# Optimization experiments

Hardware: AMD Instinct MI355X
Metric: run time of the kernel (lower is better)

Reference implementation:

```python
import jax, jax.numpy as jnp
import numpy as np

IN_FEATURES = 64 * 64 * 3  # 12288, hard-coded in the torch module

# Sign with straight-through estimator (BinaryNet-style): fwd = sign(x),
# bwd = grad * 1{|x| <= 1} (hardtanh clip).
@jax.custom_vjp
def ste_sign(x):
    return jnp.sign(x)

def _ste_fwd(x):
    return jnp.sign(x), x

def _ste_bwd(x, g):
    return (g * (jnp.abs(x) <= 1.0).astype(g.dtype),)

ste_sign.defvjp(_ste_fwd, _ste_bwd)


def setup_inputs() -> dict:
    key = jax.random.key(0)
    k1, k2 = jax.random.split(key)
    B, C = 8192, 1000
    inp = jax.random.normal(k1, (B, IN_FEATURES), dtype=jnp.float32)
    # Linear weight init scale ~ U(-1/sqrt(fan_in), 1/sqrt(fan_in)); use scaled normal
    weight = jax.random.normal(k2, (C, IN_FEATURES), dtype=jnp.float32) * (1.0 / np.sqrt(IN_FEATURES))
    return {"input": inp, "weight": weight}


def reference(input, weight):
    x = input.reshape(-1, IN_FEATURES)
    # F.linear(sign(x), sign(W)) = sign(x) @ sign(W)^T  -> [B, num_classes]
    return jnp.einsum("bd,cd->bc", ste_sign(x), ste_sign(weight))
```

## Files before the change

### kernel.cpp

```cpp
#include <hip/hip_runtime.h>
#include <hip/hip_bf16.h>


#define K_DIM   12288
#define N_CLS   1000
#define N_PAD   1024
#define KSPLIT  2
#define K_HALF  (K_DIM / KSPLIT)
#define STAGE_BYTES (N_PAD * 64)
#define N_STAGE_TOT (K_DIM / 64)
#define CHUNK_STAGES 2
#define CHUNK_K  (CHUNK_STAGES * 64)
#define CHUNKS   (K_HALF / CHUNK_K)
#define M_TILE   64
#define B_ROWS   8192
#define WS_W_BYTES ((size_t)N_STAGE_TOT * STAGE_BYTES)
#define WS_P_BYTES ((size_t)B_ROWS * N_CLS * 4)

typedef int int4v __attribute__((ext_vector_type(4)));
typedef unsigned int uint4v __attribute__((ext_vector_type(4)));

__device__ __forceinline__ unsigned sign_byte(unsigned bits) {
    unsigned mag = bits & 0x7fffffffu;
    unsigned nz = mag ? 1u : 0u;
    int sgn = ((int)bits) >> 31;
    int v = (((int)nz) ^ sgn) - sgn;
    return (unsigned)(v & 0xff);
}

__device__ __forceinline__ unsigned pack4(uint4v b) {
    return sign_byte(b.x) | (sign_byte(b.y) << 8) |
           (sign_byte(b.z) << 16) | (sign_byte(b.w) << 24);
}

__global__ void pack_w_kernel(const float* __restrict__ w,
                              unsigned char* __restrict__ ws) {
    const int gid = blockIdx.x * 256 + threadIdx.x;
    const int stage = gid >> 12;
    const int n = (gid >> 2) & 1023;
    const int q16 = gid & 3;
    const int k = stage * 64 + q16 * 16;
    uint4v o = {0u, 0u, 0u, 0u};
    if (n < N_CLS) {
        const float* p = w + (size_t)n * K_DIM + k;
        o.x = pack4(*reinterpret_cast<const uint4v*>(p));
        o.y = pack4(*reinterpret_cast<const uint4v*>(p + 4));
        o.z = pack4(*reinterpret_cast<const uint4v*>(p + 8));
        o.w = pack4(*reinterpret_cast<const uint4v*>(p + 12));
    }
    *reinterpret_cast<uint4v*>(ws + (size_t)stage * STAGE_BYTES + n * 64 + q16 * 16) = o;
}

__global__ void zero_kernel(float* __restrict__ out) {
    const int i = blockIdx.x * 256 + threadIdx.x;
    float4 z = {0.f, 0.f, 0.f, 0.f};
    *reinterpret_cast<float4*>(out + (size_t)i * 4) = z;
}

__global__ void reduce_kernel(const unsigned* __restrict__ part,
                              float* __restrict__ out) {
    const int i = blockIdx.x * 256 + threadIdx.x;
    uint4v w = *reinterpret_cast<const uint4v*>(part + (size_t)i * 4);
    float4 f;
    f.x = (float)((int)(short)(w.x & 0xffffu) + (int)(short)(w.x >> 16));
    f.y = (float)((int)(short)(w.y & 0xffffu) + (int)(short)(w.y >> 16));
    f.z = (float)((int)(short)(w.z & 0xffffu) + (int)(short)(w.z >> 16));
    f.w = (float)((int)(short)(w.w & 0xffffu) + (int)(short)(w.w >> 16));
    *reinterpret_cast<float4*>(out + (size_t)i * 4) = f;
}

template<int USE_PARTIAL>
__global__ __launch_bounds__(512, 2)
void bgemm_kernel(const float* __restrict__ x,
                  const unsigned char* __restrict__ wq,
                  unsigned* __restrict__ part,
                  float* __restrict__ out) {
    __shared__ unsigned x_lds[2][M_TILE * 32];

    const int tid  = threadIdx.x;
    const int wave = tid >> 6;
    const int lane = tid & 63;
    const int q    = lane >> 4;
    const int l15  = lane & 15;
    const int bx   = blockIdx.x;
    const int mtile = bx >> 1;
    const int kh    = bx & 1;
    const int m0    = mtile * M_TILE;
    const int nbase = wave * 128;

    int4v acc[4][8];
#pragma unroll
    for (int i = 0; i < 4; ++i)
#pragma unroll
        for (int j = 0; j < 8; ++j)
            acc[i][j] = (int4v){0, 0, 0, 0};

    const int srow = tid >> 3;
    const int scol = tid & 7;
    const float* xp = x + (size_t)(m0 + srow) * K_DIM + kh * K_HALF + scol * 4;
    const int sw_w = (srow & 3) * 8;

    const unsigned char* wqb = wq + (size_t)(kh * (N_STAGE_TOT / KSPLIT)) * STAGE_BYTES
                               + (nbase + l15) * 64 + q * 16;
    const int rsw = (l15 & 3) * 8;

    uint4v xr[4];
#pragma unroll
    for (int i = 0; i < 4; ++i)
        xr[i] = __builtin_nontemporal_load(reinterpret_cast<const uint4v*>(xp + i * 32));
#pragma unroll
    for (int i = 0; i < 4; ++i)
        x_lds[0][srow * 32 + (((i * 8 + scol)) ^ sw_w)] = pack4(xr[i]);
    __syncthreads();

#pragma unroll 2
    for (int c = 0; c < CHUNKS; ++c) {
        const int cur = c & 1;
        if (c + 1 < CHUNKS) {
            const float* xpc = xp + (size_t)(c + 1) * CHUNK_K;
#pragma unroll
            for (int i = 0; i < 4; ++i)
                xr[i] = __builtin_nontemporal_load(reinterpret_cast<const uint4v*>(xpc + i * 32));
        }
        const unsigned char* wpc = wqb + (size_t)(c * CHUNK_STAGES) * STAGE_BYTES;
#pragma unroll
        for (int st = 0; st < CHUNK_STAGES; ++st) {
            int4v a[4];
#pragma unroll
            for (int mt = 0; mt < 4; ++mt)
                a[mt] = *reinterpret_cast<const int4v*>(
                    &x_lds[cur][(mt * 16 + l15) * 32 + ((st * 16 + q * 4) ^ rsw)]);
            const unsigned char* wp = wpc + st * STAGE_BYTES;
#pragma unroll
            for (int nt = 0; nt < 8; ++nt) {
                int4v b = *reinterpret_cast<const int4v*>(wp + nt * 1024);
#pragma unroll
                for (int mt = 0; mt < 4; ++mt)
                    acc[mt][nt] = __builtin_amdgcn_mfma_i32_16x16x64_i8(a[mt], b, acc[mt][nt], 0, 0, 0);
            }
        }
        if (c + 1 < CHUNKS) {
#pragma unroll
            for (int i = 0; i < 4; ++i)
                x_lds[cur ^ 1][srow * 32 + (((i * 8 + scol)) ^ sw_w)] = pack4(xr[i]);
        }
        __syncthreads();
    }

#pragma unroll
    for (int mt = 0; mt < 4; ++mt) {
#pragma unroll
        for (int nt = 0; nt < 8; ++nt) {
            const int col = nbase + nt * 16 + l15;
            if (col < N_CLS) {
#pragma unroll
                for (int r = 0; r < 4; ++r) {
                    const int row = m0 + mt * 16 + q * 4 + r;
                    const size_t idx = (size_t)row * N_CLS + col;
                    if (USE_PARTIAL) {
                        reinterpret_cast<short*>(part)[idx * 2 + kh] = (short)acc[mt][nt][r];
                    } else {
                        atomicAdd(&out[idx], (float)acc[mt][nt][r]);
                    }
                }
            }
        }
    }
}

extern "C" void kernel_launch(void* const* d_in, const int* in_sizes, int n_in,
                              void* d_out, int out_size, void* d_ws, size_t ws_size,
                              hipStream_t stream) {
    const float* x = (const float*)d_in[0];
    const float* w = (const float*)d_in[1];
    float* out = (float*)d_out;
    unsigned char* ws = (unsigned char*)d_ws;

    pack_w_kernel<<<3072, 256, 0, stream>>>(w, ws);

    unsigned* part = reinterpret_cast<unsigned*>(ws + WS_W_BYTES);
    const bool use_part = ws_size >= WS_W_BYTES + WS_P_BYTES;
    if (use_part) {
        bgemm_kernel<1><<<256, 512, 0, stream>>>(x, ws, part, out);
        reduce_kernel<<<(B_ROWS * N_CLS) / (4 * 256), 256, 0, stream>>>(part, out);
    } else {
        zero_kernel<<<(B_ROWS * N_CLS) / (4 * 256), 256, 0, stream>>>(out);
        bgemm_kernel<0><<<256, 512, 0, stream>>>(x, ws, part, out);
    }
}
```

Before: 662.3 us.

## Use 128-row M tiles with N split across blocks and vectorized LDS stores

Doubles the M tile to 128 rows and splits the 1024 padded classes into two 512-wide halves across blocks, so each wave now computes 8x4 MFMA tiles instead of 4x8. Each thread loads 32 contiguous floats of x and writes the packed int8 signs to LDS as two 16-byte stores under a new XOR swizzle, and the loads no longer use nontemporal hints. The aim is better reuse of each weight fragment against more x rows and fewer, wider LDS writes. The trade-off is that every x tile is now read twice (once per N half), which adds global traffic.

Measured after the change: 720.3 us. 1.09x slower.

```diff
diff --git a/kernel.cpp b/kernel.cpp
--- a/kernel.cpp
+++ b/kernel.cpp
@@ -12,7 +12,7 @@
 #define CHUNK_STAGES 2
 #define CHUNK_K  (CHUNK_STAGES * 64)
 #define CHUNKS   (K_HALF / CHUNK_K)
-#define M_TILE   64
+#define M_TILE   128
 #define B_ROWS   8192
 #define WS_W_BYTES ((size_t)N_STAGE_TOT * STAGE_BYTES)
 #define WS_P_BYTES ((size_t)B_ROWS * N_CLS * 4)
@@ -83,34 +83,44 @@
     const int q    = lane >> 4;
     const int l15  = lane & 15;
     const int bx   = blockIdx.x;
-    const int mtile = bx >> 1;
-    const int kh    = bx & 1;
+    const int ns    = bx >> 7;
+    const int rem   = bx & 127;
+    const int mtile = rem >> 1;
+    const int kh    = rem & 1;
     const int m0    = mtile * M_TILE;
-    const int nbase = wave * 128;
-
-    int4v acc[4][8];
-#pragma unroll
-    for (int i = 0; i < 4; ++i)
-#pragma unroll
-        for (int j = 0; j < 8; ++j)
+    const int nbase = ns * 512 + wave * 64;
+
+    int4v acc[8][4];
+#pragma unroll
+    for (int i = 0; i < 8; ++i)
+#pragma unroll
+        for (int j = 0; j < 4; ++j)
             acc[i][j] = (int4v){0, 0, 0, 0};
 
-    const int srow = tid >> 3;
-    const int scol = tid & 7;
-    const float* xp = x + (size_t)(m0 + srow) * K_DIM + kh * K_HALF + scol * 4;
-    const int sw_w = (srow & 3) * 8;
+    const int srow = tid >> 2;
+    const int scol = tid & 3;
+    const float* xp = x + (size_t)(m0 + srow) * K_DIM + kh * K_HALF + scol * 32;
+    const int swsh = (srow & 7) * 4;
+    const int wb0  = srow * 32 + ((scol * 8 + 0) ^ swsh);
+    const int wb1  = srow * 32 + ((scol * 8 + 4) ^ swsh);
 
     const unsigned char* wqb = wq + (size_t)(kh * (N_STAGE_TOT / KSPLIT)) * STAGE_BYTES
                                + (nbase + l15) * 64 + q * 16;
-    const int rsw = (l15 & 3) * 8;
-
-    uint4v xr[4];
-#pragma unroll
-    for (int i = 0; i < 4; ++i)
-        xr[i] = __builtin_nontemporal_load(reinterpret_cast<const uint4v*>(xp + i * 32));
-#pragma unroll
-    for (int i = 0; i < 4; ++i)
-        x_lds[0][srow * 32 + (((i * 8 + scol)) ^ sw_w)] = pack4(xr[i]);
+    const int rsw = (l15 & 7) * 4;
+
+    uint4v xr[8];
+#pragma unroll
+    for (int i = 0; i < 8; ++i)
+        xr[i] = *reinterpret_cast<const uint4v*>(xp + i * 4);
+    {
+        unsigned pk[8];
+#pragma unroll
+        for (int i = 0; i < 8; ++i) pk[i] = pack4(xr[i]);
+        int4v v0 = {(int)pk[0], (int)pk[1], (int)pk[2], (int)pk[3]};
+        int4v v1 = {(int)pk[4], (int)pk[5], (int)pk[6], (int)pk[7]};
+        *reinterpret_cast<int4v*>(&x_lds[0][wb0]) = v0;
+        *reinterpret_cast<int4v*>(&x_lds[0][wb1]) = v1;
+    }
     __syncthreads();
 
 #pragma unroll 2
@@ -119,38 +129,42 @@
         if (c + 1 < CHUNKS) {
             const float* xpc = xp + (size_t)(c + 1) * CHUNK_K;
 #pragma unroll
-            for (int i = 0; i < 4; ++i)
-                xr[i] = __builtin_nontemporal_load(reinterpret_cast<const uint4v*>(xpc + i * 32));
+            for (int i = 0; i < 8; ++i)
+                xr[i] = *reinterpret_cast<const uint4v*>(xpc + i * 4);
         }
         const unsigned char* wpc = wqb + (size_t)(c * CHUNK_STAGES) * STAGE_BYTES;
 #pragma unroll
         for (int st = 0; st < CHUNK_STAGES; ++st) {
-            int4v a[4];
-#pragma unroll
-            for (int mt = 0; mt < 4; ++mt)
+            int4v a[8];
+#pragma unroll
+            for (int mt = 0; mt < 8; ++mt)
                 a[mt] = *reinterpret_cast<const int4v*>(
                     &x_lds[cur][(mt * 16 + l15) * 32 + ((st * 16 + q * 4) ^ rsw)]);
             const unsigned char* wp = wpc + st * STAGE_BYTES;
 #pragma unroll
-            for (int nt = 0; nt < 8; ++nt) {
+            for (int nt = 0; nt < 4; ++nt) {
                 int4v b = *reinterpret_cast<const int4v*>(wp + nt * 1024);
 #pragma unroll
-                for (int mt = 0; mt < 4; ++mt)
+                for (int mt = 0; mt < 8; ++mt)
                     acc[mt][nt] = __builtin_amdgcn_mfma_i32_16x16x64_i8(a[mt], b, acc[mt][nt], 0, 0, 0);
             }
         }
         if (c + 1 < CHUNKS) {
-#pragma unroll
-            for (int i = 0; i < 4; ++i)
-                x_lds[cur ^ 1][srow * 32 + (((i * 8 + scol)) ^ sw_w)] = pack4(xr[i]);
+            unsigned pk[8];
+#pragma unroll
+            for (int i = 0; i < 8; ++i) pk[i] = pack4(xr[i]);
+            int4v v0 = {(int)pk[0], (int)pk[1], (int)pk[2], (int)pk[3]};
+            int4v v1 = {(int)pk[4], (int)pk[5], (int)pk[6], (int)pk[7]};
+            *reinterpret_cast<int4v*>(&x_lds[cur ^ 1][wb0]) = v0;
+            *reinterpret_cast<int4v*>(&x_lds[cur ^ 1][wb1]) = v1;
         }
         __syncthreads();
     }
 
 #pragma unroll
-    for (int mt = 0; mt < 4; ++mt) {
-#pragma unroll
-        for (int nt = 0; nt < 8; ++nt) {
+    for (int mt = 0; mt < 8; ++mt) {
+#pragma unroll
+        for (int nt = 0; nt < 4; ++nt) {
             const int col = nbase + nt * 16 + l15;
             if (col < N_CLS) {
 #pragma unroll
```
